# Optimization experiments

Hardware: AMD Instinct MI355X
Metric: run time of the kernel (lower is better)

The kernel has to match this reference:

```python
import jax, jax.numpy as jnp
import numpy as np

N_NODES = 50000
N_EDGES = 800000
NEG_SLOPE = 0.2  # leaky_relu slope used in the model


def setup_inputs() -> dict:
    key = jax.random.key(0)
    ks = jax.random.split(key, 8)
    d_in, d_h, d_out = 64, 64, 4
    x = jax.random.normal(ks[0], (N_NODES, d_in), dtype=jnp.float32)
    edge_index = jax.random.randint(ks[1], (2, N_EDGES), 0, N_NODES, dtype=jnp.int32)
    # Glorot-style init like PyG GCNConv
    W0 = jax.random.normal(ks[2], (d_in, d_h), dtype=jnp.float32) * np.float32(1.0 / np.sqrt(d_in))
    W1 = jax.random.normal(ks[3], (d_h, d_h), dtype=jnp.float32) * np.float32(1.0 / np.sqrt(d_h))
    W2 = jax.random.normal(ks[4], (d_h, d_out), dtype=jnp.float32) * np.float32(1.0 / np.sqrt(d_h))
    b0 = jnp.zeros((d_h,), dtype=jnp.float32)
    b1 = jnp.zeros((d_h,), dtype=jnp.float32)
    b2 = jnp.zeros((d_out,), dtype=jnp.float32)
    return {"x": x, "edge_index": edge_index, "W0": W0, "b0": b0,
            "W1": W1, "b1": b1, "W2": W2, "b2": b2}


def _gcn_norm(edge_index, n_nodes, dtype):
    # Add self-loops, compute symmetric normalization D^{-1/2} (A+I) D^{-1/2}
    src, dst = edge_index[0], edge_index[1]
    loop = jnp.arange(n_nodes, dtype=src.dtype)
    src = jnp.concatenate([src, loop])
    dst = jnp.concatenate([dst, loop])
    deg = jax.ops.segment_sum(jnp.ones_like(dst, dtype=dtype), dst, num_segments=n_nodes)
    dinv = jnp.where(deg > 0, jax.lax.rsqrt(deg), jnp.zeros_like(deg))
    norm = dinv[src] * dinv[dst]  # [E + N]
    return src, dst, norm


def _gcn_layer(h, src, dst, norm, W, b, n_nodes):
    h = h @ W                                  # [N, d_out]
    msg = h[src] * norm[:, None]               # gather + edge scaling
    out = jax.ops.segment_sum(msg, dst, num_segments=n_nodes)  # scatter-add
    return out + b


def reference(x, edge_index, W0, b0, W1, b1, W2, b2):
    # Eval-mode forward: dropout_edge and F.dropout are identity when not training.
    n = x.shape[0]
    src, dst, norm = _gcn_norm(edge_index, n, x.dtype)
    h = _gcn_layer(x, src, dst, norm, W0, b0, n)
    h = jax.nn.leaky_relu(h, NEG_SLOPE)
    h = _gcn_layer(h, src, dst, norm, W1, b1, n)
    h = jax.nn.leaky_relu(h, NEG_SLOPE)
    out = _gcn_layer(h, src, dst, norm, W2, b2, n)
    return out
```

## Files before the change

### kernel.cpp

```cpp
#include <hip/hip_runtime.h>
#include <math.h>

#define NEG_SLOPE 0.2f
#define NPAD 50176
#define NW8  (NPAD / 4)
#define NCHUNK 128

typedef _Float16 half4 __attribute__((ext_vector_type(4)));

__global__ __launch_bounds__(1024) void k_hist(const int* __restrict__ dst,
                                               unsigned int* __restrict__ histw,
                                               int e, int es) {
    extern __shared__ unsigned int lcnt[];
    int t = threadIdx.x;
    for (int w = t; w < NW8; w += 1024) lcnt[w] = 0u;
    __syncthreads();
    int beg = blockIdx.x * es;
    int end = min(beg + es, e);
    for (int i = beg + t; i < end; i += 1024) {
        int d = dst[i];
        atomicAdd(&lcnt[d >> 2], 1u << ((d & 3) << 3));
    }
    __syncthreads();
    unsigned int* out = histw + (size_t)blockIdx.x * NW8;
    for (int w = t; w < NW8; w += 1024) out[w] = lcnt[w];
}

__global__ __launch_bounds__(256) void k_chscan(unsigned char* __restrict__ hist8,
                                                float* __restrict__ dinv,
                                                unsigned short* __restrict__ deg16,
                                                int* __restrict__ bsum, int n) {
    int t = threadIdx.x;
    int i = blockIdx.x * 256 + t;
    unsigned char* p = hist8 + i;
    unsigned int run = 0;
    for (int c = 0; c < NCHUNK; c += 8) {
        size_t b = (size_t)c * NPAD;
        unsigned char v0 = p[b];
        unsigned char v1 = p[b + (size_t)1 * NPAD];
        unsigned char v2 = p[b + (size_t)2 * NPAD];
        unsigned char v3 = p[b + (size_t)3 * NPAD];
        unsigned char v4 = p[b + (size_t)4 * NPAD];
        unsigned char v5 = p[b + (size_t)5 * NPAD];
        unsigned char v6 = p[b + (size_t)6 * NPAD];
        unsigned char v7 = p[b + (size_t)7 * NPAD];
        unsigned int e0 = run;
        unsigned int e1 = e0 + v0;
        unsigned int e2 = e1 + v1;
        unsigned int e3 = e2 + v2;
        unsigned int e4 = e3 + v3;
        unsigned int e5 = e4 + v4;
        unsigned int e6 = e5 + v5;
        unsigned int e7 = e6 + v6;
        run = e7 + v7;
        p[b] = (unsigned char)e0;
        p[b + (size_t)1 * NPAD] = (unsigned char)e1;
        p[b + (size_t)2 * NPAD] = (unsigned char)e2;
        p[b + (size_t)3 * NPAD] = (unsigned char)e3;
        p[b + (size_t)4 * NPAD] = (unsigned char)e4;
        p[b + (size_t)5 * NPAD] = (unsigned char)e5;
        p[b + (size_t)6 * NPAD] = (unsigned char)e6;
        p[b + (size_t)7 * NPAD] = (unsigned char)e7;
    }
    int deg = (int)run;
    if (i < n) dinv[i] = rsqrtf((float)(deg + 1));
    deg16[i] = (unsigned short)deg;
    int s = deg;
    for (int d = 1; d < 64; d <<= 1) s += __shfl_down(s, d);
    __shared__ int ws[4];
    if ((t & 63) == 0) ws[t >> 6] = s;
    __syncthreads();
    if (t == 0) bsum[blockIdx.x] = ws[0] + ws[1] + ws[2] + ws[3];
}

__global__ __launch_bounds__(256) void k_scan3(const unsigned short* __restrict__ deg16,
                                               const int* __restrict__ bsum,
                                               int* __restrict__ rowptr, int n, int nb) {
    __shared__ int ls[256];
    __shared__ int wo[4];
    int t = threadIdx.x;
    int bid = blockIdx.x;
    int bv = (t < bid && t < nb) ? bsum[t] : 0;
    for (int d = 1; d < 64; d <<= 1) bv += __shfl_down(bv, d);
    if ((t & 63) == 0) wo[t >> 6] = bv;
    __syncthreads();
    int boff = wo[0] + wo[1] + wo[2] + wo[3];
    int i = bid * 256 + t;
    int v = (i < n) ? (int)deg16[i] : 0;
    ls[t] = v;
    __syncthreads();
    for (int d = 1; d < 256; d <<= 1) {
        int u = (t >= d) ? ls[t - d] : 0;
        __syncthreads();
        ls[t] += u;
        __syncthreads();
    }
    int excl = ls[t] - v + boff;
    if (i < n) rowptr[i] = excl;
    if (i == n - 1) rowptr[n] = excl + v;
}

__global__ __launch_bounds__(1024) void k_place2(const int* __restrict__ src,
                                                 const int* __restrict__ dst,
                                                 const int* __restrict__ rowptr,
                                                 const unsigned int* __restrict__ choffw,
                                                 int* __restrict__ perm, int e, int es) {
    extern __shared__ unsigned int cur[];
    int t = threadIdx.x;
    const unsigned int* in = choffw + (size_t)blockIdx.x * NW8;
    for (int w = t; w < NW8; w += 1024) cur[w] = in[w];
    __syncthreads();
    int beg = blockIdx.x * es;
    int end = min(beg + es, e);
    for (int i = beg + t; i < end; i += 1024) {
        int d = dst[i];
        int sh = (d & 3) << 3;
        unsigned int old = atomicAdd(&cur[d >> 2], 1u << sh);
        int slot = rowptr[d] + (int)((old >> sh) & 0xffu);
        perm[slot] = src[i];
    }
}

__global__ __launch_bounds__(256) void k_gemm64(const float* __restrict__ in,
                                                const float* __restrict__ W,
                                                const float* __restrict__ dinv,
                                                _Float16* __restrict__ out, int n) {
    __shared__ float Ws[64 * 64];
    __shared__ float Xs[16 * 64];
    int t = threadIdx.x;
    const float4* W4 = (const float4*)W;
    float4* Ws4 = (float4*)Ws;
#pragma unroll
    for (int i = 0; i < 4; ++i) Ws4[t + 256 * i] = W4[t + 256 * i];
    int row0 = blockIdx.x * 16;
    {
        int r = t >> 4, c4 = t & 15;
        int row = row0 + r;
        float4 v = make_float4(0.f, 0.f, 0.f, 0.f);
        if (row < n) v = ((const float4*)(in + (size_t)row * 64))[c4];
        ((float4*)Xs)[t] = v;
    }
    __syncthreads();
    int c = t & 63, g = t >> 6;
    float a0 = 0.f, a1 = 0.f, a2 = 0.f, a3 = 0.f;
#pragma unroll
    for (int k = 0; k < 64; ++k) {
        float w = Ws[k * 64 + c];
        a0 = fmaf(Xs[g * 64 + k], w, a0);
        a1 = fmaf(Xs[(g + 4) * 64 + k], w, a1);
        a2 = fmaf(Xs[(g + 8) * 64 + k], w, a2);
        a3 = fmaf(Xs[(g + 12) * 64 + k], w, a3);
    }
    int r;
    r = row0 + g;      if (r < n) out[(size_t)r * 64 + c] = (_Float16)(a0 * dinv[r]);
    r = row0 + g + 4;  if (r < n) out[(size_t)r * 64 + c] = (_Float16)(a1 * dinv[r]);
    r = row0 + g + 8;  if (r < n) out[(size_t)r * 64 + c] = (_Float16)(a2 * dinv[r]);
    r = row0 + g + 12; if (r < n) out[(size_t)r * 64 + c] = (_Float16)(a3 * dinv[r]);
}

__global__ __launch_bounds__(512) void k_gather_gemm(
        const _Float16* __restrict__ h, const float* __restrict__ dinv,
        const int* __restrict__ rowptr, const int* __restrict__ perm,
        const float* __restrict__ b, const float* __restrict__ W,
        _Float16* __restrict__ out, int n) {
    __shared__ float Ws[64 * 64];
    __shared__ float Xs[8 * 64];
    int t = threadIdx.x;
    ((float4*)Ws)[t] = ((const float4*)W)[t];
    ((float4*)Ws)[t + 512] = ((const float4*)W)[t + 512];
    int row0 = blockIdx.x * 8;
    int wid = t >> 6;
    int lane = t & 63;
    int v = row0 + wid;
    if (v < n) {
        v = __builtin_amdgcn_readfirstlane(v);
        const _Float16* hl = h + lane;
        float acc = (float)hl[(size_t)v * 64];
        int e = rowptr[v], end = rowptr[v + 1];
#define LOADK(j) float x##j = (float)hl[(size_t)perm[e + j] * 64]
        for (; e + 16 <= end; e += 16) {
            LOADK(0); LOADK(1); LOADK(2); LOADK(3);
            LOADK(4); LOADK(5); LOADK(6); LOADK(7);
            LOADK(8); LOADK(9); LOADK(10); LOADK(11);
            LOADK(12); LOADK(13); LOADK(14); LOADK(15);
            acc += (((x0 + x1) + (x2 + x3)) + ((x4 + x5) + (x6 + x7)))
                 + (((x8 + x9) + (x10 + x11)) + ((x12 + x13) + (x14 + x15)));
        }
        if (e + 8 <= end) {
            LOADK(0); LOADK(1); LOADK(2); LOADK(3);
            LOADK(4); LOADK(5); LOADK(6); LOADK(7);
            acc += ((x0 + x1) + (x2 + x3)) + ((x4 + x5) + (x6 + x7));
            e += 8;
        }
        if (e + 4 <= end) {
            LOADK(0); LOADK(1); LOADK(2); LOADK(3);
            acc += (x0 + x1) + (x2 + x3);
            e += 4;
        }
        if (e + 2 <= end) {
            LOADK(0); LOADK(1);
            acc += x0 + x1;
            e += 2;
        }
        if (e < end) acc += (float)hl[(size_t)perm[e] * 64];
#undef LOADK
        float dv = dinv[v];
        acc = acc * dv + b[lane];
        acc = acc > 0.0f ? acc : acc * NEG_SLOPE;
        Xs[wid * 64 + lane] = acc;
    }
    __syncthreads();
    {
        int c = lane, g = wid;
        float a0 = 0.f;
#pragma unroll
        for (int k = 0; k < 64; ++k)
            a0 = fmaf(Xs[g * 64 + k], Ws[k * 64 + c], a0);
        int r = row0 + g;
        if (r < n) out[(size_t)r * 64 + c] = (_Float16)(a0 * dinv[r]);
    }
}

__global__ __launch_bounds__(256) void k_gather64(
        const _Float16* __restrict__ h, const float* __restrict__ dinv,
        const int* __restrict__ rowptr, const int* __restrict__ perm,
        const float* __restrict__ b, int n,
        const float* __restrict__ W2, float* __restrict__ y) {
    int t = threadIdx.x;
    int v = blockIdx.x * 4 + (t >> 6);
    if (v >= n) return;
    v = __builtin_amdgcn_readfirstlane(v);
    int lane = t & 63;
    const _Float16* hl = h + lane;
    float acc = (float)hl[(size_t)v * 64];
    int e = rowptr[v], end = rowptr[v + 1];
#define LOADK(j) float x##j = (float)hl[(size_t)perm[e + j] * 64]
    for (; e + 16 <= end; e += 16) {
        LOADK(0); LOADK(1); LOADK(2); LOADK(3);
        LOADK(4); LOADK(5); LOADK(6); LOADK(7);
        LOADK(8); LOADK(9); LOADK(10); LOADK(11);
        LOADK(12); LOADK(13); LOADK(14); LOADK(15);
        acc += (((x0 + x1) + (x2 + x3)) + ((x4 + x5) + (x6 + x7)))
             + (((x8 + x9) + (x10 + x11)) + ((x12 + x13) + (x14 + x15)));
    }
    if (e + 8 <= end) {
        LOADK(0); LOADK(1); LOADK(2); LOADK(3);
        LOADK(4); LOADK(5); LOADK(6); LOADK(7);
        acc += ((x0 + x1) + (x2 + x3)) + ((x4 + x5) + (x6 + x7));
        e += 8;
    }
    if (e + 4 <= end) {
        LOADK(0); LOADK(1); LOADK(2); LOADK(3);
        acc += (x0 + x1) + (x2 + x3);
        e += 4;
    }
    if (e + 2 <= end) {
        LOADK(0); LOADK(1);
        acc += x0 + x1;
        e += 2;
    }
    if (e < end) acc += (float)hl[(size_t)perm[e] * 64];
#undef LOADK
    float dv = dinv[v];
    acc = acc * dv + b[lane];
    acc = acc > 0.0f ? acc : acc * NEG_SLOPE;
    float4 w = ((const float4*)W2)[lane];
    float p0 = acc * w.x, p1 = acc * w.y, p2 = acc * w.z, p3 = acc * w.w;
#pragma unroll
    for (int dlt = 1; dlt < 64; dlt <<= 1) {
        p0 += __shfl_xor(p0, dlt);
        p1 += __shfl_xor(p1, dlt);
        p2 += __shfl_xor(p2, dlt);
        p3 += __shfl_xor(p3, dlt);
    }
    if (lane == 0)
        ((float4*)y)[v] = make_float4(p0 * dv, p1 * dv, p2 * dv, p3 * dv);
}

__global__ __launch_bounds__(256) void k_gather4(
        const float* __restrict__ h, const float* __restrict__ dinv,
        const int* __restrict__ rowptr, const int* __restrict__ perm,
        const float* __restrict__ b, float* __restrict__ out, int n) {
    int gid = blockIdx.x * 256 + threadIdx.x;
    int c = gid & 3;
    int v = gid >> 2;
    if (v >= n) return;
    const float* hc = h + c;
    float acc = hc[(size_t)v * 4];
    int e = rowptr[v], end = rowptr[v + 1];
    for (; e + 4 <= end; e += 4) {
        float x0 = hc[(size_t)perm[e] * 4];
        float x1 = hc[(size_t)perm[e + 1] * 4];
        float x2 = hc[(size_t)perm[e + 2] * 4];
        float x3 = hc[(size_t)perm[e + 3] * 4];
        acc += (x0 + x1) + (x2 + x3);
    }
    for (; e < end; ++e) acc += hc[(size_t)perm[e] * 4];
    out[(size_t)v * 4 + c] = acc * dinv[v] + b[c];
}

extern "C" void kernel_launch(void* const* d_in, const int* in_sizes, int n_in,
                              void* d_out, int out_size, void* d_ws, size_t ws_size,
                              hipStream_t stream) {
    const float* x  = (const float*)d_in[0];
    const int* ei   = (const int*)d_in[1];
    const float* W0 = (const float*)d_in[2];
    const float* b0 = (const float*)d_in[3];
    const float* W1 = (const float*)d_in[4];
    const float* b1 = (const float*)d_in[5];
    const float* W2 = (const float*)d_in[6];
    const float* b2 = (const float*)d_in[7];
    float* out = (float*)d_out;

    const int N = in_sizes[0] / 64;
    const int E = in_sizes[1] / 2;
    const int* src = ei;
    const int* dst = ei + E;
    const int es = (E + NCHUNK - 1) / NCHUNK;

    char* base = (char*)d_ws;
    size_t off = 0;
    auto alloc = [&](size_t bytes) { size_t o = off; off = (off + bytes + 255) & ~(size_t)255; return o; };
    unsigned int*   histw  = (unsigned int*)(base + alloc((size_t)NCHUNK * NPAD));
    unsigned short* deg16  = (unsigned short*)(base + alloc((size_t)NPAD * 2));
    float*          dinv   = (float*)(base + alloc((size_t)NPAD * 4));
    int*            rowptr = (int*)(base + alloc((size_t)(NPAD + 1) * 4));
    int*            bsum   = (int*)(base + alloc(1024));
    int*            perm   = (int*)(base + alloc((size_t)E * 4));
    _Float16*       bufH   = (_Float16*)(base + alloc((size_t)N * 64 * 2));
    _Float16*       bufH2  = (_Float16*)(base + alloc((size_t)N * 64 * 2));
    float*          bufD   = (float*)(base + alloc((size_t)N * 4 * 4));

    const int nb_N = (N + 255) / 256;
    const int nb_V = (N + 3) / 4;

    k_hist<<<NCHUNK, 1024, NW8 * sizeof(unsigned int), stream>>>(dst, histw, E, es);
    k_chscan<<<NPAD / 256, 256, 0, stream>>>((unsigned char*)histw, dinv, deg16, bsum, N);
    k_scan3<<<nb_N, 256, 0, stream>>>(deg16, bsum, rowptr, N, nb_N);
    k_place2<<<NCHUNK, 1024, NW8 * sizeof(unsigned int), stream>>>(src, dst, rowptr, histw, perm, E, es);

    k_gemm64<<<(N + 15) / 16, 256, 0, stream>>>(x, W0, dinv, bufH, N);

    k_gather_gemm<<<(N + 7) / 8, 512, 0, stream>>>(bufH, dinv, rowptr, perm, b0, W1, bufH2, N);

    k_gather64<<<nb_V, 256, 0, stream>>>(bufH2, dinv, rowptr, perm, b1, N, W2, bufD);

    k_gather4<<<(N * 4 + 255) / 256, 256, 0, stream>>>(bufD, dinv, rowptr, perm, b2, out, N);
}
```

Baseline: 135.9 us.

## Fuse chunk scan and row-pointer scan using decoupled look-back

Merges the per-chunk histogram scan kernel and the separate block-offset scan kernel into one kernel. Each block publishes its aggregate to a look-back array with status flags and waits on its predecessors to get its exclusive offset. This removes one kernel launch and the deg16/bsum round trip through global memory. In exchange it depends on blocks being scheduled in forward order, since later blocks spin on earlier ones, and it adds serial spinning in thread 0.

```diff
diff --git a/kernel.cpp b/kernel.cpp
--- a/kernel.cpp
+++ b/kernel.cpp
@@ -10,9 +10,11 @@
 
 __global__ __launch_bounds__(1024) void k_hist(const int* __restrict__ dst,
                                                unsigned int* __restrict__ histw,
+                                               unsigned int* __restrict__ look,
                                                int e, int es) {
     extern __shared__ unsigned int lcnt[];
     int t = threadIdx.x;
+    if (blockIdx.x == 0 && t < 256) look[t] = 0u;
     for (int w = t; w < NW8; w += 1024) lcnt[w] = 0u;
     __syncthreads();
     int beg = blockIdx.x * es;
@@ -26,12 +28,15 @@
     for (int w = t; w < NW8; w += 1024) out[w] = lcnt[w];
 }
 
-__global__ __launch_bounds__(256) void k_chscan(unsigned char* __restrict__ hist8,
-                                                float* __restrict__ dinv,
-                                                unsigned short* __restrict__ deg16,
-                                                int* __restrict__ bsum, int n) {
-    int t = threadIdx.x;
-    int i = blockIdx.x * 256 + t;
+__global__ __launch_bounds__(256) void k_chscan3(unsigned char* __restrict__ hist8,
+                                                 float* __restrict__ dinv,
+                                                 unsigned int* __restrict__ look,
+                                                 int* __restrict__ rowptr, int n) {
+    __shared__ int ls[256];
+    __shared__ int sboff;
+    int t = threadIdx.x;
+    int bid = blockIdx.x;
+    int i = bid * 256 + t;
     unsigned char* p = hist8 + i;
     unsigned int run = 0;
     for (int c = 0; c < NCHUNK; c += 8) {
@@ -62,32 +67,9 @@
         p[b + (size_t)6 * NPAD] = (unsigned char)e6;
         p[b + (size_t)7 * NPAD] = (unsigned char)e7;
     }
-    int deg = (int)run;
+    int deg = (i < n) ? (int)run : 0;
     if (i < n) dinv[i] = rsqrtf((float)(deg + 1));
-    deg16[i] = (unsigned short)deg;
-    int s = deg;
-    for (int d = 1; d < 64; d <<= 1) s += __shfl_down(s, d);
-    __shared__ int ws[4];
-    if ((t & 63) == 0) ws[t >> 6] = s;
-    __syncthreads();
-    if (t == 0) bsum[blockIdx.x] = ws[0] + ws[1] + ws[2] + ws[3];
-}
-
-__global__ __launch_bounds__(256) void k_scan3(const unsigned short* __restrict__ deg16,
-                                               const int* __restrict__ bsum,
-                                               int* __restrict__ rowptr, int n, int nb) {
-    __shared__ int ls[256];
-    __shared__ int wo[4];
-    int t = threadIdx.x;
-    int bid = blockIdx.x;
-    int bv = (t < bid && t < nb) ? bsum[t] : 0;
-    for (int d = 1; d < 64; d <<= 1) bv += __shfl_down(bv, d);
-    if ((t & 63) == 0) wo[t >> 6] = bv;
-    __syncthreads();
-    int boff = wo[0] + wo[1] + wo[2] + wo[3];
-    int i = bid * 256 + t;
-    int v = (i < n) ? (int)deg16[i] : 0;
-    ls[t] = v;
+    ls[t] = deg;
     __syncthreads();
     for (int d = 1; d < 256; d <<= 1) {
         int u = (t >= d) ? ls[t - d] : 0;
@@ -95,9 +77,23 @@
         ls[t] += u;
         __syncthreads();
     }
-    int excl = ls[t] - v + boff;
+    if (t == 0) {
+        int total = ls[255];
+        atomicExch(&look[bid], (unsigned int)total | (1u << 30));
+        int boff = 0;
+        for (int j = bid - 1; j >= 0; --j) {
+            unsigned int v;
+            do { v = atomicAdd(&look[j], 0u); } while ((v >> 30) == 0u);
+            boff += (int)(v & 0x00FFFFFFu);
+            if ((v >> 30) == 2u) break;
+        }
+        atomicExch(&look[bid], (unsigned int)(total + boff) | (2u << 30));
+        sboff = boff;
+    }
+    __syncthreads();
+    int excl = ls[t] - deg + sboff;
     if (i < n) rowptr[i] = excl;
-    if (i == n - 1) rowptr[n] = excl + v;
+    if (i == n - 1) rowptr[n] = excl + deg;
 }
 
 __global__ __launch_bounds__(1024) void k_place2(const int* __restrict__ src,
@@ -322,21 +318,18 @@
     size_t off = 0;
     auto alloc = [&](size_t bytes) { size_t o = off; off = (off + bytes + 255) & ~(size_t)255; return o; };
     unsigned int*   histw  = (unsigned int*)(base + alloc((size_t)NCHUNK * NPAD));
-    unsigned short* deg16  = (unsigned short*)(base + alloc((size_t)NPAD * 2));
     float*          dinv   = (float*)(base + alloc((size_t)NPAD * 4));
     int*            rowptr = (int*)(base + alloc((size_t)(NPAD + 1) * 4));
-    int*            bsum   = (int*)(base + alloc(1024));
+    unsigned int*   look   = (unsigned int*)(base + alloc(1024));
     int*            perm   = (int*)(base + alloc((size_t)E * 4));
     _Float16*       bufH   = (_Float16*)(base + alloc((size_t)N * 64 * 2));
     _Float16*       bufH2  = (_Float16*)(base + alloc((size_t)N * 64 * 2));
     float*          bufD   = (float*)(base + alloc((size_t)N * 4 * 4));
 
-    const int nb_N = (N + 255) / 256;
     const int nb_V = (N + 3) / 4;
 
-    k_hist<<<NCHUNK, 1024, NW8 * sizeof(unsigned int), stream>>>(dst, histw, E, es);
-    k_chscan<<<NPAD / 256, 256, 0, stream>>>((unsigned char*)histw, dinv, deg16, bsum, N);
-    k_scan3<<<nb_N, 256, 0, stream>>>(deg16, bsum, rowptr, N, nb_N);
+    k_hist<<<NCHUNK, 1024, NW8 * sizeof(unsigned int), stream>>>(dst, histw, look, E, es);
+    k_chscan3<<<NPAD / 256, 256, 0, stream>>>((unsigned char*)histw, dinv, look, rowptr, N);
     k_place2<<<NCHUNK, 1024, NW8 * sizeof(unsigned int), stream>>>(src, dst, rowptr, histw, perm, E, es);
 
     k_gemm64<<<(N + 15) / 16, 256, 0, stream>>>(x, W0, dinv, bufH, N);
```

After: 144.8 us. 1.07x slower.
